# Performance work log

Hardware: AMD Instinct MI355X
Metric: run time of the kernel (lower is better)

The kernel has to match this reference:

```python
import jax, jax.numpy as jnp
import numpy as np

S_DIM, I_DIM, O_DIM = 1024, 2048, 1024
TOTAL = S_DIM + I_DIM + O_DIM  # 4096
INPUT_DIM, NUM_CLASSES, BATCH = 2048, 1000, 256


def setup_inputs() -> dict:
    key = jax.random.key(0)
    ks = jax.random.split(key, 6)
    x = jax.random.normal(ks[0], (BATCH, INPUT_DIM), dtype=jnp.float32)
    W = jax.random.normal(ks[1], (TOTAL, TOTAL), dtype=jnp.float32) * 0.02
    # torch Linear: weight [out, in], bias [out]
    in_w = jax.random.normal(ks[2], (S_DIM, INPUT_DIM), dtype=jnp.float32) * (1.0 / np.sqrt(INPUT_DIM))
    in_b = jax.random.normal(ks[3], (S_DIM,), dtype=jnp.float32) * 0.01
    out_w = jax.random.normal(ks[4], (NUM_CLASSES, O_DIM), dtype=jnp.float32) * (1.0 / np.sqrt(O_DIM))
    out_b = jax.random.normal(ks[5], (NUM_CLASSES,), dtype=jnp.float32) * 0.01
    return {"x": x, "W": W, "in_w": in_w, "in_b": in_b, "out_w": out_w, "out_b": out_b, "time_steps": 10}


def reference(x, W, in_w, in_b, out_w, out_b, time_steps):
    B = x.shape[0]
    S, I, O = S_DIM, I_DIM, O_DIM
    # slice effective W into 9 sub-blocks (use_lora=False -> W_eff = W)
    W_ss, W_sr, W_so = W[:S, :S], W[:S, S:S + I], W[:S, S + I:]
    W_rs, W_rr, W_ro = W[S:S + I, :S], W[S:S + I, S:S + I], W[S:S + I, S + I:]
    W_os, W_or, W_oo = W[S + I:, :S], W[S + I:, S:S + I], W[S + I:, S + I:]

    E = x @ in_w.T + in_b  # [B, S]
    gate = (jnp.arange(time_steps) % 5 == 0).astype(x.dtype)  # E injected when t%5==0

    init = (jnp.zeros((B, S), x.dtype), jnp.zeros((B, I), x.dtype), jnp.zeros((B, O), x.dtype))

    def step(carry, g):
        Ss, Is, Os = carry
        S_next = jax.nn.relu(Ss @ W_ss + g * E + Is @ W_rs + Os @ W_os)
        I_next = jax.nn.relu(Is @ W_rr + Ss @ W_sr + Os @ W_or)
        O_next = jax.nn.relu(Os @ W_oo + Is @ W_ro + Ss @ W_so)
        return (S_next, I_next, O_next), None

    (Ss, Is, Os), _ = jax.lax.scan(step, init, gate)
    return Os @ out_w.T + out_b  # [B, num_classes]
```

## Files before the change

kernel.cpp:

```cpp
#include <hip/hip_runtime.h>


typedef __bf16 bf16x8 __attribute__((ext_vector_type(8)));
typedef float  f32x16 __attribute__((ext_vector_type(16)));

#define TOTAL 4096
#define BATCH 256
#define INDIM 2048
#define SDIM  1024
#define NCLS  1000

#define MFMA(a, b, c) __builtin_amdgcn_mfma_f32_32x32x16_bf16((a), (b), (c), 0, 0, 0)

__device__ inline f32x16 zero16() {
    f32x16 v;
#pragma unroll
    for (int i = 0; i < 16; ++i) v[i] = 0.f;
    return v;
}

__device__ inline void swz_slot(const float* __restrict__ in, __bf16* __restrict__ out,
                                int C, int Rvalid, int t) {
    const int lane = t & 63;
    const int frag = t >> 6;
    const int kcN = C >> 4;
    const int rt = frag / kcN;
    const int kc = frag - rt * kcN;
    const int r = rt * 32 + (lane & 31);
    const int c = kc * 16 + (lane >> 5) * 8;
    alignas(16) __bf16 v[8];
    if (r < Rvalid) {
        const float* p = in + (size_t)r * C + c;
#pragma unroll
        for (int j = 0; j < 8; ++j) v[j] = (__bf16)p[j];
    } else {
#pragma unroll
        for (int j = 0; j < 8; ++j) v[j] = (__bf16)0.f;
    }
    *(ulonglong2*)(out + (size_t)t * 8) = *(const ulonglong2*)v;
}

__global__ __launch_bounds__(256) void k_prep(const float* __restrict__ W,
                                              const float* __restrict__ x,
                                              const float* __restrict__ in_w,
                                              const float* __restrict__ in_b,
                                              const float* __restrict__ out_w,
                                              __bf16* __restrict__ WT,
                                              __bf16* __restrict__ OWT,
                                              float* __restrict__ Ebuf,
                                              __bf16* __restrict__ H0) {
    __shared__ float t[16 * 512];
    const int bid = blockIdx.x;
    const int tid = threadIdx.x;
    if (bid < 256) {
        float* red = t;
        const int mt = bid >> 5, nt = bid & 31;
        const int wave = tid >> 6, lane = tid & 63;
        const int l31 = lane & 31, kh = (lane >> 5) * 8;
        const int k0 = wave * 512;
        const float* Ax = x    + (size_t)(mt * 32 + l31) * INDIM + k0 + kh;
        const float* Bw = in_w + (size_t)(nt * 32 + l31) * INDIM + k0 + kh;
        f32x16 acc = zero16();
#pragma unroll 4
        for (int i = 0; i < 32; ++i) {
            const float* pa = Ax + i * 16;
            const float* pb = Bw + i * 16;
            float4 a0 = *(const float4*)pa, a1 = *(const float4*)(pa + 4);
            float4 b0 = *(const float4*)pb, b1 = *(const float4*)(pb + 4);
            bf16x8 a, b;
            a[0] = (__bf16)a0.x; a[1] = (__bf16)a0.y; a[2] = (__bf16)a0.z; a[3] = (__bf16)a0.w;
            a[4] = (__bf16)a1.x; a[5] = (__bf16)a1.y; a[6] = (__bf16)a1.z; a[7] = (__bf16)a1.w;
            b[0] = (__bf16)b0.x; b[1] = (__bf16)b0.y; b[2] = (__bf16)b0.z; b[3] = (__bf16)b0.w;
            b[4] = (__bf16)b1.x; b[5] = (__bf16)b1.y; b[6] = (__bf16)b1.z; b[7] = (__bf16)b1.w;
            acc = MFMA(a, b, acc);
        }
#pragma unroll
        for (int r = 0; r < 16; ++r) {
            int row = (r & 3) + 8 * (r >> 2) + 4 * (lane >> 5);
            red[wave * 1024 + row * 32 + l31] = acc[r];
        }
        __syncthreads();
        const int e0 = tid * 4;
        float4 s = {0.f, 0.f, 0.f, 0.f};
#pragma unroll
        for (int w = 0; w < 4; ++w) {
            float4 v = *(const float4*)&red[w * 1024 + e0];
            s.x += v.x; s.y += v.y; s.z += v.z; s.w += v.w;
        }
        const int row = e0 >> 5, col = e0 & 31;
        const int m = mt * 32 + row, n = nt * 32 + col;
        float v[4] = {s.x + in_b[n], s.y + in_b[n + 1], s.z + in_b[n + 2], s.w + in_b[n + 3]};
        *(float4*)(Ebuf + m * SDIM + n) = *(const float4*)v;
        alignas(8) __bf16 o[4];
#pragma unroll
        for (int j = 0; j < 4; ++j) o[j] = (__bf16)fmaxf(v[j], 0.f);
        const size_t frag = (size_t)(m >> 5) * (TOTAL / 16) + (n >> 4);
        const int lh = (m & 31) + 32 * ((n >> 3) & 1);
        *(ushort4*)(H0 + frag * 512 + lh * 8 + (n & 7)) = *(const ushort4*)o;
    } else if (bid < 2304) {
        const int wb = bid - 256;
        const int k0 = (wb >> 3) * 16;
        const int n0 = (wb & 7) * 512;
#pragma unroll
        for (int i = 0; i < 8; ++i) {
            const int slot = i * 256 + tid;
            const int row = slot >> 7;
            const int c4 = (slot & 127) * 4;
            float4 v = *(const float4*)(W + (size_t)(k0 + row) * TOTAL + n0 + c4);
            *(float4*)&t[row * 512 + c4] = v;
        }
        __syncthreads();
        const int kcG = k0 >> 4;
#pragma unroll
        for (int s = tid; s < 1024; s += 256) {
            const int rtl = s >> 6;
            const int lane = s & 63;
            const int nl = rtl * 32 + (lane & 31);
            const int kl = (lane >> 5) * 8;
            bf16x8 v;
#pragma unroll
            for (int j = 0; j < 8; ++j) v[j] = (__bf16)t[(kl + j) * 512 + nl];
            const size_t fragG = (size_t)((n0 >> 5) + rtl) * (TOTAL / 16) + kcG;
            *(bf16x8*)(WT + fragG * 512 + lane * 8) = v;
        }
    } else {
        swz_slot(out_w, OWT, 1024, NCLS, (bid - 2304) * 256 + tid);
    }
}

template <int CHUNKS>
__global__ __launch_bounds__(512, 2) void k_step(const __bf16* __restrict__ h,
                                                 const __bf16* __restrict__ WT,
                                                 const float* __restrict__ E,
                                                 const int gate,
                                                 __bf16* __restrict__ hn) {
    __shared__ float buf[4][4096];
    const int wave = threadIdx.x >> 6;
    const int lane = threadIdx.x & 63;
    const int xcd = blockIdx.x & 7;
    const int idx = blockIdx.x >> 3;
    const int mt = idx & 3;
    const int nt = xcd * 8 + (idx >> 2);
    constexpr int PER = CHUNKS >> 3;
    const int kc0 = wave * PER;

    const bf16x8* A0 = (const bf16x8*)h  + ((size_t)(mt * 2) * (TOTAL / 16) + kc0) * 64 + lane;
    const bf16x8* A1 = A0 + (size_t)(TOTAL / 16) * 64;
    const bf16x8* B0 = (const bf16x8*)WT + ((size_t)(nt * 2) * (TOTAL / 16) + kc0) * 64 + lane;
    const bf16x8* B1 = B0 + (size_t)(TOTAL / 16) * 64;

    f32x16 ac0 = zero16(), ac1 = zero16(), ac2 = zero16(), ac3 = zero16();
#pragma unroll 4
    for (int i = 0; i < PER; ++i) {
        const int off = i * 64;
        bf16x8 a0 = A0[off];
        bf16x8 a1 = A1[off];
        bf16x8 b0 = B0[off];
        bf16x8 b1 = B1[off];
        ac0 = MFMA(a0, b0, ac0);
        ac1 = MFMA(a0, b1, ac1);
        ac2 = MFMA(a1, b0, ac2);
        ac3 = MFMA(a1, b1, ac3);
    }

    f32x16 accs[4] = {ac0, ac1, ac2, ac3};
    if (wave >= 4) {
        float* b = buf[wave - 4];
#pragma unroll
        for (int c = 0; c < 4; ++c)
#pragma unroll
            for (int r = 0; r < 16; ++r)
                b[(c * 16 + r) * 64 + lane] = accs[c][r];
    }
    __syncthreads();
    if (wave < 4) {
        float* b = buf[wave];
#pragma unroll
        for (int c = 0; c < 4; ++c)
#pragma unroll
            for (int r = 0; r < 16; ++r) {
                const int i2 = (c * 16 + r) * 64 + lane;
                b[i2] += accs[c][r];
            }
    }
    __syncthreads();

    const int t = threadIdx.x;
    const int c = t >> 7;
    const int r = (t >> 3) & 15;
    const int l0 = (t & 7) * 8;
    const int base = (c * 16 + r) * 64 + l0;
    float4 s0 = {0.f, 0.f, 0.f, 0.f}, s1 = {0.f, 0.f, 0.f, 0.f};
#pragma unroll
    for (int w = 0; w < 4; ++w) {
        const float4* p = (const float4*)&buf[w][base];
        float4 v0 = p[0], v1 = p[1];
        s0.x += v0.x; s0.y += v0.y; s0.z += v0.z; s0.w += v0.w;
        s1.x += v1.x; s1.y += v1.y; s1.z += v1.z; s1.w += v1.w;
    }
    float v[8] = {s0.x, s0.y, s0.z, s0.w, s1.x, s1.y, s1.z, s1.w};
    const int ih = c >> 1, jh = c & 1;
    const int row = ih * 32 + (r & 3) + 8 * (r >> 2) + 4 * (l0 >> 5);
    const int col0 = jh * 32 + (l0 & 31);
    const int m = mt * 64 + row;
    const int n0g = nt * 64 + col0;
    if (gate && n0g < SDIM) {
        const float* Ep = E + m * SDIM + n0g;
#pragma unroll
        for (int j = 0; j < 8; ++j) v[j] += Ep[j];
    }
    alignas(16) __bf16 o[8];
#pragma unroll
    for (int j = 0; j < 8; ++j) o[j] = (__bf16)fmaxf(v[j], 0.f);
    const size_t frag = (size_t)(m >> 5) * (TOTAL / 16) + (n0g >> 4);
    const int lh = (m & 31) + 32 * ((n0g >> 3) & 1);
    *(ulonglong2*)(hn + frag * 512 + lh * 8) = *(const ulonglong2*)o;
}

__global__ __launch_bounds__(512, 2) void k_part9(const __bf16* __restrict__ h,
                                                  const __bf16* __restrict__ WT,
                                                  float* __restrict__ P) {
    __shared__ float buf[4][4096];
    const int wave = threadIdx.x >> 6;
    const int lane = threadIdx.x & 63;
    const int xcd = blockIdx.x & 7;
    const int idx = blockIdx.x >> 3;
    const int nt = 48 + xcd * 2 + (idx >> 4);
    const int mt = (idx >> 2) & 3;
    const int ks = idx & 3;
    const int kc0 = ks * 64 + wave * 8;

    const bf16x8* A0 = (const bf16x8*)h  + ((size_t)(mt * 2) * (TOTAL / 16) + kc0) * 64 + lane;
    const bf16x8* A1 = A0 + (size_t)(TOTAL / 16) * 64;
    const bf16x8* B0 = (const bf16x8*)WT + ((size_t)(nt * 2) * (TOTAL / 16) + kc0) * 64 + lane;
    const bf16x8* B1 = B0 + (size_t)(TOTAL / 16) * 64;

    f32x16 ac0 = zero16(), ac1 = zero16(), ac2 = zero16(), ac3 = zero16();
#pragma unroll 4
    for (int i = 0; i < 8; ++i) {
        const int off = i * 64;
        bf16x8 a0 = A0[off];
        bf16x8 a1 = A1[off];
        bf16x8 b0 = B0[off];
        bf16x8 b1 = B1[off];
        ac0 = MFMA(a0, b0, ac0);
        ac1 = MFMA(a0, b1, ac1);
        ac2 = MFMA(a1, b0, ac2);
        ac3 = MFMA(a1, b1, ac3);
    }

    f32x16 accs[4] = {ac0, ac1, ac2, ac3};
    if (wave >= 4) {
        float* b = buf[wave - 4];
#pragma unroll
        for (int c = 0; c < 4; ++c)
#pragma unroll
            for (int r = 0; r < 16; ++r)
                b[(c * 16 + r) * 64 + lane] = accs[c][r];
    }
    __syncthreads();
    if (wave < 4) {
        float* b = buf[wave];
#pragma unroll
        for (int c = 0; c < 4; ++c)
#pragma unroll
            for (int r = 0; r < 16; ++r) {
                const int i2 = (c * 16 + r) * 64 + lane;
                b[i2] += accs[c][r];
            }
    }
    __syncthreads();

    const int t = threadIdx.x;
    const int c = t >> 7;
    const int r = (t >> 3) & 15;
    const int l0 = (t & 7) * 8;
    const int base = (c * 16 + r) * 64 + l0;
    float4 s0 = {0.f, 0.f, 0.f, 0.f}, s1 = {0.f, 0.f, 0.f, 0.f};
#pragma unroll
    for (int w = 0; w < 4; ++w) {
        const float4* p = (const float4*)&buf[w][base];
        float4 v0 = p[0], v1 = p[1];
        s0.x += v0.x; s0.y += v0.y; s0.z += v0.z; s0.w += v0.w;
        s1.x += v1.x; s1.y += v1.y; s1.z += v1.z; s1.w += v1.w;
    }
    alignas(16) float v[8] = {s0.x, s0.y, s0.z, s0.w, s1.x, s1.y, s1.z, s1.w};
    const int ih = c >> 1, jh = c & 1;
    const int row = ih * 32 + (r & 3) + 8 * (r >> 2) + 4 * (l0 >> 5);
    const int col0 = jh * 32 + (l0 & 31);
    const int m = mt * 64 + row;
    const int nl = (nt - 48) * 64 + col0;
    float* p = P + ((size_t)ks << 18) + (size_t)m * 1024 + nl;
    *(float4*)p = *(const float4*)&v[0];
    *(float4*)(p + 4) = *(const float4*)&v[4];
}

__global__ __launch_bounds__(256) void k_red9(const float* __restrict__ P,
                                              __bf16* __restrict__ hn) {
    const int g = blockIdx.x * 256 + threadIdx.x;
    const int m = g >> 7;
    const int n8 = (g & 127) << 3;
    const float* p = P + (size_t)m * 1024 + n8;
    float4 a0 = *(const float4*)p, a1 = *(const float4*)(p + 4);
#pragma unroll
    for (int ks = 1; ks < 4; ++ks) {
        const float* q = p + ((size_t)ks << 18);
        float4 b0 = *(const float4*)q, b1 = *(const float4*)(q + 4);
        a0.x += b0.x; a0.y += b0.y; a0.z += b0.z; a0.w += b0.w;
        a1.x += b1.x; a1.y += b1.y; a1.z += b1.z; a1.w += b1.w;
    }
    alignas(16) __bf16 o[8];
    o[0] = (__bf16)fmaxf(a0.x, 0.f); o[1] = (__bf16)fmaxf(a0.y, 0.f);
    o[2] = (__bf16)fmaxf(a0.z, 0.f); o[3] = (__bf16)fmaxf(a0.w, 0.f);
    o[4] = (__bf16)fmaxf(a1.x, 0.f); o[5] = (__bf16)fmaxf(a1.y, 0.f);
    o[6] = (__bf16)fmaxf(a1.z, 0.f); o[7] = (__bf16)fmaxf(a1.w, 0.f);
    const int n0g = 3072 + n8;
    const size_t frag = (size_t)(m >> 5) * (TOTAL / 16) + (n0g >> 4);
    const int lh = (m & 31) + 32 * ((n0g >> 3) & 1);
    *(ulonglong2*)(hn + frag * 512 + lh * 8) = *(const ulonglong2*)o;
}

__global__ __launch_bounds__(512, 4) void k_out(const __bf16* __restrict__ h,
                                                const __bf16* __restrict__ owt,
                                                const float* __restrict__ out_b,
                                                float* __restrict__ out) {
    __shared__ float red[8][1024];
    const int wave = threadIdx.x >> 6;
    const int lane = threadIdx.x & 63;
    const int mt = blockIdx.x >> 5;
    const int ct = blockIdx.x & 31;
    const int m0 = mt * 32, c0 = ct * 32;
    const int kcA0 = (3072 / 16) + wave * 8;
    const int kcB0 = wave * 8;
    const bf16x8* Ap = (const bf16x8*)h   + ((size_t)mt * (TOTAL / 16) + kcA0) * 64 + lane;
    const bf16x8* Bp = (const bf16x8*)owt + ((size_t)ct * (1024 / 16) + kcB0) * 64 + lane;
    f32x16 acc = zero16();
#pragma unroll
    for (int i = 0; i < 8; ++i)
        acc = MFMA(Ap[i * 64], Bp[i * 64], acc);
#pragma unroll
    for (int r = 0; r < 16; ++r) {
        int row = (r & 3) + 8 * (r >> 2) + 4 * (lane >> 5);
        red[wave][row * 32 + (lane & 31)] = acc[r];
    }
    __syncthreads();
    const int e0 = threadIdx.x * 2;
    float sx = 0.f, sy = 0.f;
#pragma unroll
    for (int w = 0; w < 8; ++w) {
        float2 v = *(const float2*)&red[w][e0];
        sx += v.x; sy += v.y;
    }
    const int row = e0 >> 5, col = e0 & 31;
    const int m = m0 + row;
    const int n = c0 + col;
    if (n < NCLS)     out[m * NCLS + n]     = sx + out_b[n];
    if (n + 1 < NCLS) out[m * NCLS + n + 1] = sy + out_b[n + 1];
}

extern "C" void kernel_launch(void* const* d_in, const int* in_sizes, int n_in,
                              void* d_out, int out_size, void* d_ws, size_t ws_size,
                              hipStream_t stream) {
    const float* x     = (const float*)d_in[0];
    const float* W     = (const float*)d_in[1];
    const float* in_w  = (const float*)d_in[2];
    const float* in_b  = (const float*)d_in[3];
    const float* out_w = (const float*)d_in[4];
    const float* out_b = (const float*)d_in[5];
    float* out = (float*)d_out;

    char* ws = (char*)d_ws;
    __bf16* WT  = (__bf16*)(ws + 0);
    __bf16* OWT = (__bf16*)(ws + 33554432);
    float*  Ebuf= (float*)(ws + 35651584);
    __bf16* H0  = (__bf16*)(ws + 36700160);
    __bf16* H1  = (__bf16*)(ws + 38797312);
    float*  Pbuf= (float*)(ws + 40894464);

    k_prep<<<2816, 256, 0, stream>>>(W, x, in_w, in_b, out_w, WT, OWT, Ebuf, H0);

    const __bf16* hs = H0;
    __bf16* hd = H1;
    for (int t = 1; t < 9; ++t) {
        const int gate = (t % 5 == 0) ? 1 : 0;
        if (t == 1)
            k_step<SDIM / 16><<<256, 512, 0, stream>>>(hs, WT, Ebuf, gate, hd);
        else
            k_step<TOTAL / 16><<<256, 512, 0, stream>>>(hs, WT, Ebuf, gate, hd);
        const __bf16* tmp = hs; hs = hd; hd = (__bf16*)tmp;
    }

    k_part9<<<256, 512, 0, stream>>>(hs, WT, Pbuf);
    k_red9<<<128, 256, 0, stream>>>(Pbuf, hd);

    k_out<<<256, 512, 0, stream>>>(hd, OWT, out_b, out);
}
```

Measured before the change: 259.2 us.

## Split recurrent steps into split-K LDS-staged GEMM plus separate reduction kernel

Replaces the fused full-K step kernel for timesteps 2-8 with a split-K GEMM (four K slices, 128x128 tiles, 1024 threads) that stages A and B fragments into double-buffered LDS via global_load_lds. A separate reduction kernel then sums the four partial fp32 slabs, adds the gated input, applies ReLU and writes bf16 in fragment layout. The goal is better parallelism and load overlap per step. The cost is an extra launch per step plus writing and re-reading 16 MB of fp32 partials each step.

```diff
diff --git a/kernel.cpp b/kernel.cpp
--- a/kernel.cpp
+++ b/kernel.cpp
@@ -17,6 +17,13 @@
 #pragma unroll
     for (int i = 0; i < 16; ++i) v[i] = 0.f;
     return v;
+}
+
+__device__ inline void gload_lds16(const void* g, void* l) {
+    __builtin_amdgcn_global_load_lds(
+        (__attribute__((address_space(1))) void*)(const_cast<void*>(g)),
+        (__attribute__((address_space(3))) void*)l,
+        16, 0, 0);
 }
 
 __device__ inline void swz_slot(const float* __restrict__ in, __bf16* __restrict__ out,
@@ -217,6 +224,102 @@
     *(ulonglong2*)(hn + frag * 512 + lh * 8) = *(const ulonglong2*)o;
 }
 
+__global__ __launch_bounds__(1024) void k_step2(const __bf16* __restrict__ h,
+                                                const __bf16* __restrict__ WT,
+                                                float* __restrict__ P) {
+    __shared__ __bf16 sm[2][64 * 512];
+    const int tid = threadIdx.x;
+    const int w = tid >> 6;
+    const int lane = tid & 63;
+    const int xcd = blockIdx.x & 7;
+    const int idx = blockIdx.x >> 3;
+    const int ks = xcd >> 1;
+    const int nt = (xcd & 1) * 16 + (idx >> 1);
+    const int mt = idx & 1;
+    const int rm = w >> 2, rn = w & 3;
+    const int kb = ks * 64;
+
+    auto stage = [&](int b, int c) {
+        const int kc = kb + c * 8;
+#pragma unroll
+        for (int i = 0; i < 4; ++i) {
+            const int f = w * 4 + i;
+            const void* src;
+            if (f < 32) {
+                src = (const void*)(h + ((size_t)((mt * 4 + (f >> 3)) * (TOTAL / 16) + kc + (f & 7))) * 512 + lane * 8);
+            } else {
+                const int fb = f - 32;
+                src = (const void*)(WT + ((size_t)((nt * 4 + (fb >> 3)) * (TOTAL / 16) + kc + (fb & 7))) * 512 + lane * 8);
+            }
+            gload_lds16(src, (void*)&sm[b][f * 512]);
+        }
+    };
+
+    f32x16 acc = zero16();
+    int buf = 0;
+    stage(0, 0);
+    __syncthreads();
+#pragma unroll 2
+    for (int c = 0; c < 8; ++c) {
+        if (c + 1 < 8) stage(buf ^ 1, c + 1);
+        const __bf16* As = &sm[buf][(rm * 8) * 512];
+        const __bf16* Bs = &sm[buf][(32 + rn * 8) * 512];
+        bf16x8 a[8], b[8];
+#pragma unroll
+        for (int fk = 0; fk < 8; ++fk) {
+            a[fk] = *(const bf16x8*)(As + fk * 512 + lane * 8);
+            b[fk] = *(const bf16x8*)(Bs + fk * 512 + lane * 8);
+        }
+#pragma unroll
+        for (int fk = 0; fk < 8; ++fk) acc = MFMA(a[fk], b[fk], acc);
+        __syncthreads();
+        buf ^= 1;
+    }
+
+    const int m0 = mt * 128 + rm * 32;
+    const int n0 = nt * 128 + rn * 32;
+    const int col = lane & 31;
+    const int rb = 4 * (lane >> 5);
+    float* Pp = P + (size_t)ks * (BATCH * TOTAL) + (size_t)m0 * TOTAL + n0 + col;
+#pragma unroll
+    for (int r = 0; r < 16; ++r) {
+        const int row = (r & 3) + 8 * (r >> 2) + rb;
+        Pp[(size_t)row * TOTAL] = acc[r];
+    }
+}
+
+__global__ __launch_bounds__(256) void k_red2(const float* __restrict__ P,
+                                              const float* __restrict__ E,
+                                              const int gate,
+                                              __bf16* __restrict__ hn) {
+    const int g = blockIdx.x * 256 + threadIdx.x;
+    const int m = g >> 9;
+    const int n8 = (g & 511) << 3;
+    const float* p = P + (size_t)m * TOTAL + n8;
+    float4 a0 = *(const float4*)p, a1 = *(const float4*)(p + 4);
+#pragma unroll
+    for (int s = 1; s < 4; ++s) {
+        const float* q = p + (size_t)s * (BATCH * TOTAL);
+        float4 b0 = *(const float4*)q, b1 = *(const float4*)(q + 4);
+        a0.x += b0.x; a0.y += b0.y; a0.z += b0.z; a0.w += b0.w;
+        a1.x += b1.x; a1.y += b1.y; a1.z += b1.z; a1.w += b1.w;
+    }
+    if (gate && n8 < SDIM) {
+        const float* Ep = E + (size_t)m * SDIM + n8;
+        float4 e0 = *(const float4*)Ep, e1 = *(const float4*)(Ep + 4);
+        a0.x += e0.x; a0.y += e0.y; a0.z += e0.z; a0.w += e0.w;
+        a1.x += e1.x; a1.y += e1.y; a1.z += e1.z; a1.w += e1.w;
+    }
+    alignas(16) __bf16 o[8];
+    o[0] = (__bf16)fmaxf(a0.x, 0.f); o[1] = (__bf16)fmaxf(a0.y, 0.f);
+    o[2] = (__bf16)fmaxf(a0.z, 0.f); o[3] = (__bf16)fmaxf(a0.w, 0.f);
+    o[4] = (__bf16)fmaxf(a1.x, 0.f); o[5] = (__bf16)fmaxf(a1.y, 0.f);
+    o[6] = (__bf16)fmaxf(a1.z, 0.f); o[7] = (__bf16)fmaxf(a1.w, 0.f);
+    const size_t frag = (size_t)(m >> 5) * (TOTAL / 16) + (n8 >> 4);
+    const int lh = (m & 31) + 32 * ((n8 >> 3) & 1);
+    *(ulonglong2*)(hn + frag * 512 + lh * 8) = *(const ulonglong2*)o;
+}
+
 __global__ __launch_bounds__(512, 2) void k_part9(const __bf16* __restrict__ h,
                                                   const __bf16* __restrict__ WT,
                                                   float* __restrict__ P) {
@@ -381,12 +484,13 @@
 
     const __bf16* hs = H0;
     __bf16* hd = H1;
-    for (int t = 1; t < 9; ++t) {
-        const int gate = (t % 5 == 0) ? 1 : 0;
-        if (t == 1)
-            k_step<SDIM / 16><<<256, 512, 0, stream>>>(hs, WT, Ebuf, gate, hd);
-        else
-            k_step<TOTAL / 16><<<256, 512, 0, stream>>>(hs, WT, Ebuf, gate, hd);
+
+    k_step<SDIM / 16><<<256, 512, 0, stream>>>(hs, WT, Ebuf, 0, hd);
+    { const __bf16* tmp = hs; hs = hd; hd = (__bf16*)tmp; }
+
+    for (int t = 2; t < 9; ++t) {
+        k_step2<<<256, 1024, 0, stream>>>(hs, WT, Pbuf);
+        k_red2<<<512, 256, 0, stream>>>(Pbuf, Ebuf, (t % 5 == 0) ? 1 : 0, hd);
         const __bf16* tmp = hs; hs = hd; hd = (__bf16*)tmp;
     }
 
```

Result: slower. 295.0 us (+13.8%).

## Split step-kernel K reduction across 16 waves with 1024-thread blocks

Applied to the files above, without the earlier changes.

The recurrent step kernel now launches 1024 threads per block and splits the K dimension across 16 waves instead of 8, halving per-wave MFMA work. Partial accumulators are reduced through an 8-slot shared buffer (128 KB of LDS), and the epilogue writes 4 bf16 values per thread instead of 8. The intent is more waves in flight per CU to hide global-load latency in this latency-bound step. In exchange it needs more LDS and a longer cross-wave reduction, and only one block fits per CU.

```diff
diff --git a/kernel.cpp b/kernel.cpp
--- a/kernel.cpp
+++ b/kernel.cpp
@@ -129,20 +129,20 @@
 }
 
 template <int CHUNKS>
-__global__ __launch_bounds__(512, 2) void k_step(const __bf16* __restrict__ h,
-                                                 const __bf16* __restrict__ WT,
-                                                 const float* __restrict__ E,
-                                                 const int gate,
-                                                 __bf16* __restrict__ hn) {
-    __shared__ float buf[4][4096];
-    const int wave = threadIdx.x >> 6;
+__global__ __launch_bounds__(1024, 1) void k_step3(const __bf16* __restrict__ h,
+                                                   const __bf16* __restrict__ WT,
+                                                   const float* __restrict__ E,
+                                                   const int gate,
+                                                   __bf16* __restrict__ hn) {
+    __shared__ float buf[8][4096];
+    const int w = threadIdx.x >> 6;
     const int lane = threadIdx.x & 63;
     const int xcd = blockIdx.x & 7;
     const int idx = blockIdx.x >> 3;
     const int mt = idx & 3;
     const int nt = xcd * 8 + (idx >> 2);
-    constexpr int PER = CHUNKS >> 3;
-    const int kc0 = wave * PER;
+    constexpr int PER = CHUNKS >> 4;
+    const int kc0 = w * PER;
 
     const bf16x8* A0 = (const bf16x8*)h  + ((size_t)(mt * 2) * (TOTAL / 16) + kc0) * 64 + lane;
     const bf16x8* A1 = A0 + (size_t)(TOTAL / 16) * 64;
@@ -164,41 +164,39 @@
     }
 
     f32x16 accs[4] = {ac0, ac1, ac2, ac3};
-    if (wave >= 4) {
-        float* b = buf[wave - 4];
-#pragma unroll
-        for (int c = 0; c < 4; ++c)
-#pragma unroll
-            for (int r = 0; r < 16; ++r)
-                b[(c * 16 + r) * 64 + lane] = accs[c][r];
-    }
-    __syncthreads();
-    if (wave < 4) {
-        float* b = buf[wave];
-#pragma unroll
-        for (int c = 0; c < 4; ++c)
-#pragma unroll
-            for (int r = 0; r < 16; ++r) {
-                const int i2 = (c * 16 + r) * 64 + lane;
-                b[i2] += accs[c][r];
+    if (w >= 8) {
+        float* b = buf[w - 8];
+#pragma unroll
+        for (int cc = 0; cc < 4; ++cc)
+#pragma unroll
+            for (int rr = 0; rr < 16; ++rr)
+                b[(cc * 16 + rr) * 64 + lane] = accs[cc][rr];
+    }
+    __syncthreads();
+    if (w < 8) {
+        float* b = buf[w];
+#pragma unroll
+        for (int cc = 0; cc < 4; ++cc)
+#pragma unroll
+            for (int rr = 0; rr < 16; ++rr) {
+                const int i2 = (cc * 16 + rr) * 64 + lane;
+                b[i2] += accs[cc][rr];
             }
     }
     __syncthreads();
 
     const int t = threadIdx.x;
-    const int c = t >> 7;
-    const int r = (t >> 3) & 15;
-    const int l0 = (t & 7) * 8;
+    const int c = t >> 8;
+    const int r = (t >> 4) & 15;
+    const int l0 = (t & 15) * 4;
     const int base = (c * 16 + r) * 64 + l0;
-    float4 s0 = {0.f, 0.f, 0.f, 0.f}, s1 = {0.f, 0.f, 0.f, 0.f};
-#pragma unroll
-    for (int w = 0; w < 4; ++w) {
-        const float4* p = (const float4*)&buf[w][base];
-        float4 v0 = p[0], v1 = p[1];
-        s0.x += v0.x; s0.y += v0.y; s0.z += v0.z; s0.w += v0.w;
-        s1.x += v1.x; s1.y += v1.y; s1.z += v1.z; s1.w += v1.w;
-    }
-    float v[8] = {s0.x, s0.y, s0.z, s0.w, s1.x, s1.y, s1.z, s1.w};
+    float4 s = {0.f, 0.f, 0.f, 0.f};
+#pragma unroll
+    for (int wb = 0; wb < 8; ++wb) {
+        float4 v0 = *(const float4*)&buf[wb][base];
+        s.x += v0.x; s.y += v0.y; s.z += v0.z; s.w += v0.w;
+    }
+    float v[4] = {s.x, s.y, s.z, s.w};
     const int ih = c >> 1, jh = c & 1;
     const int row = ih * 32 + (r & 3) + 8 * (r >> 2) + 4 * (l0 >> 5);
     const int col0 = jh * 32 + (l0 & 31);
@@ -207,14 +205,14 @@
     if (gate && n0g < SDIM) {
         const float* Ep = E + m * SDIM + n0g;
 #pragma unroll
-        for (int j = 0; j < 8; ++j) v[j] += Ep[j];
-    }
-    alignas(16) __bf16 o[8];
-#pragma unroll
-    for (int j = 0; j < 8; ++j) o[j] = (__bf16)fmaxf(v[j], 0.f);
+        for (int j = 0; j < 4; ++j) v[j] += Ep[j];
+    }
+    alignas(8) __bf16 o[4];
+#pragma unroll
+    for (int j = 0; j < 4; ++j) o[j] = (__bf16)fmaxf(v[j], 0.f);
     const size_t frag = (size_t)(m >> 5) * (TOTAL / 16) + (n0g >> 4);
     const int lh = (m & 31) + 32 * ((n0g >> 3) & 1);
-    *(ulonglong2*)(hn + frag * 512 + lh * 8) = *(const ulonglong2*)o;
+    *(ushort4*)(hn + frag * 512 + lh * 8 + (n0g & 7)) = *(const ushort4*)o;
 }
 
 __global__ __launch_bounds__(512, 2) void k_part9(const __bf16* __restrict__ h,
@@ -384,9 +382,9 @@
     for (int t = 1; t < 9; ++t) {
         const int gate = (t % 5 == 0) ? 1 : 0;
         if (t == 1)
-            k_step<SDIM / 16><<<256, 512, 0, stream>>>(hs, WT, Ebuf, gate, hd);
+            k_step3<SDIM / 16><<<256, 1024, 0, stream>>>(hs, WT, Ebuf, gate, hd);
         else
-            k_step<TOTAL / 16><<<256, 512, 0, stream>>>(hs, WT, Ebuf, gate, hd);
+            k_step3<TOTAL / 16><<<256, 1024, 0, stream>>>(hs, WT, Ebuf, gate, hd);
         const __bf16* tmp = hs; hs = hd; hd = (__bf16*)tmp;
     }
 
```

Measured after the change: 257.6 us. No clear change (-0.6%).
